# Kernel tuning notes

Measured on AMD Instinct MI355X. Metric: run time of the kernel, lower is better.

Reference implementation:

```python
import jax, jax.numpy as jnp
import numpy as np

N = 100000   # nodes
E = 1600000  # edges
FEAT = 128
HID = 128
TGT = 64
L = 3
G = 512      # graphs in batch


def setup_inputs() -> dict:
    key = jax.random.key(0)
    ks = jax.random.split(key, 16)
    s = 0.05
    return {
        "x": jax.random.normal(ks[0], (N, FEAT), jnp.float32),
        "edge_index": jax.random.randint(ks[1], (2, E), 0, N, dtype=jnp.int32),
        "batch": jnp.sort(jax.random.randint(ks[2], (N,), 0, G, dtype=jnp.int32)),
        "conv_w1": jax.random.normal(ks[3], (L, FEAT, HID), jnp.float32) * s,
        "conv_b1": jax.random.normal(ks[4], (L, HID), jnp.float32) * s,
        "conv_w2": jax.random.normal(ks[5], (L, HID, HID), jnp.float32) * s,
        "conv_b2": jax.random.normal(ks[6], (L, HID), jnp.float32) * s,
        "eps": jnp.zeros((L,), jnp.float32),
        "gn_scale": jnp.ones((L, HID), jnp.float32),
        "gn_weight": jnp.ones((L, HID), jnp.float32),
        "gn_bias": jnp.zeros((L, HID), jnp.float32),
        "proj_w1": jax.random.normal(ks[7], (L, HID, HID), jnp.float32) * s,
        "proj_b1": jax.random.normal(ks[8], (L, HID), jnp.float32) * s,
        "proj_w2": jax.random.normal(ks[9], (L, HID, TGT), jnp.float32) * s,
        "proj_b2": jax.random.normal(ks[10], (L, TGT), jnp.float32) * s,
    }


def _graph_norm(h, batch, counts, scale, weight, bias):
    # per-graph mean -> scatter back to nodes
    mean = jax.ops.segment_sum(h, batch, num_segments=G) / counts
    sub = h - mean[batch] * scale
    var = jax.ops.segment_sum(sub * sub, batch, num_segments=G) / counts
    std = jnp.sqrt(var + 1e-8)
    return weight * sub / std[batch] + bias


def reference(x, edge_index, batch, conv_w1, conv_b1, conv_w2, conv_b2, eps,
              gn_scale, gn_weight, gn_bias, proj_w1, proj_b1, proj_w2, proj_b2):
    src, dst = edge_index[0], edge_index[1]
    counts = jnp.maximum(
        jax.ops.segment_sum(jnp.ones((N, 1), x.dtype), batch, num_segments=G), 1.0)
    h = x
    z_cat = []
    for l in range(L):
        # GINConv: aggr_j->i then 2-layer MLP
        aggr = jax.ops.segment_sum(h[src], dst, num_segments=N)
        h = (1.0 + eps[l]) * h + aggr
        h = jax.nn.relu(h @ conv_w1[l] + conv_b1[l]) @ conv_w2[l] + conv_b2[l]
        # GraphNorm
        h = _graph_norm(h, batch, counts, gn_scale[l], gn_weight[l], gn_bias[l])
        h = jax.nn.relu(h)
        # projection MLP + global add pool
        z = jax.nn.relu(h @ proj_w1[l] + proj_b1[l]) @ proj_w2[l] + proj_b2[l]
        z_cat.append(jax.ops.segment_sum(z, batch, num_segments=G))
    return jnp.concatenate(z_cat, axis=-1)  # [G, L*TGT]
```

## Files before the change

### kernel.cpp

```cpp
#include <hip/hip_runtime.h>

#define NN 100000
#define EE 1600000
#define HIDD 128
#define TGTT 64
#define GGG 512
#define NBK 98
#define CAPB 17408
#define ABLK 200
#define LSTR 136
#define CVTB 3125
#define GBLK 782
#define OUTB 128

typedef unsigned short ushort_t;
typedef __attribute__((ext_vector_type(8))) short short8;
typedef __attribute__((ext_vector_type(4))) float f32x4;
typedef __attribute__((ext_vector_type(4))) unsigned short us4;

__device__ __forceinline__ float b2f(ushort_t u) {
    union { unsigned int i; float f; } v; v.i = ((unsigned int)u) << 16; return v.f;
}
__device__ __forceinline__ ushort_t f2b(float f) {
    union { float f; unsigned int i; } v; v.f = f;
    unsigned int r = (v.i + 0x7fffu + ((v.i >> 16) & 1u)) >> 16;
    return (ushort_t)r;
}

__global__ __launch_bounds__(256) void k_pro(const float* __restrict__ x, ushort_t* __restrict__ Xb,
                                             const float* __restrict__ cw1, const float* __restrict__ cw2,
                                             const float* __restrict__ pw1, ushort_t* __restrict__ Wt,
                                             const int* __restrict__ batch, int* __restrict__ goff,
                                             const int* __restrict__ ei, int* __restrict__ gcnt,
                                             unsigned int* __restrict__ bbuf) {
    __shared__ ushort_t sW[128 * 129];
    __shared__ int cnt[NBK], base[NBK], cur[NBK];
    int b = blockIdx.x, t = threadIdx.x;

    if (b < CVTB) {
        long i0 = (long)b * 1024 + t;
#pragma unroll
        for (int c = 0; c < 4; c++) {
            long i = i0 + c * 256;
            float4 v = ((const float4*)x)[i];
            us4 o; o.x = f2b(v.x); o.y = f2b(v.y); o.z = f2b(v.z); o.w = f2b(v.w);
            ((us4*)Xb)[i] = o;
        }
        return;
    }
    b -= CVTB;
    if (b < 9) {
        int l = b / 3, j = b % 3;
        const float* src = (j == 0 ? cw1 : j == 1 ? cw2 : pw1) + (size_t)l * HIDD * HIDD;
        ushort_t* dst = Wt + (size_t)b * HIDD * HIDD;
        for (int i = t; i < HIDD * HIDD; i += 256) {
            int k = i >> 7, n = i & 127;
            sW[n * 129 + k] = f2b(src[i]);
        }
        __syncthreads();
        for (int i = t; i < HIDD * HIDD; i += 256) {
            dst[i] = sW[(i >> 7) * 129 + (i & 127)];
        }
        return;
    }
    b -= 9;
    if (b < 3) {
        int g = b * 256 + t;
        if (g > GGG) return;
        int lo = 0, hi = NN;
        while (lo < hi) { int mid = (lo + hi) >> 1; if (batch[mid] < g) lo = mid + 1; else hi = mid; }
        goff[g] = lo;
        return;
    }
    b -= 3;
    {
        if (t < NBK) cnt[t] = 0;
        __syncthreads();
        int e0 = b * 8000;
        int e1 = min(e0 + 8000, EE);
        for (int e = e0 + t; e < e1; e += 256)
            atomicAdd(&cnt[ei[EE + e] >> 10], 1);
        __syncthreads();
        if (t < NBK) { base[t] = atomicAdd(&gcnt[t], cnt[t]); cur[t] = 0; }
        __syncthreads();
        for (int e = e0 + t; e < e1; e += 256) {
            int s = ei[e], d = ei[EE + e];
            int bk = d >> 10;
            int off = base[bk] + atomicAdd(&cur[bk], 1);
            if (off < CAPB)
                bbuf[(long)bk * CAPB + off] = (unsigned int)s | (((unsigned int)d & 1023u) << 17);
        }
    }
}

__global__ __launch_bounds__(256) void k_csr(const int* __restrict__ gcnt,
                                             const unsigned int* __restrict__ bbuf,
                                             int* __restrict__ rowptr, int* __restrict__ csr) {
    __shared__ int ldeg[1024], lcur[1024], tsum[256], sb[NBK];
    int b = blockIdx.x, t = threadIdx.x;
    if (t < NBK) sb[t] = gcnt[t];
    __syncthreads();
    if (t == 0) { int a = 0; for (int i = 0; i < NBK; i++) { int v = sb[i]; sb[i] = a; a += v; } }
    __syncthreads();
    int cnt = min(gcnt[b], CAPB);
    int base = sb[b];
    const unsigned int* bb = bbuf + (long)b * CAPB;
#pragma unroll
    for (int i = 0; i < 4; i++) ldeg[t + 256 * i] = 0;
    __syncthreads();
    for (int i = t; i < cnt; i += 256) atomicAdd(&ldeg[bb[i] >> 17], 1);
    __syncthreads();
    int d0 = ldeg[4 * t], d1 = ldeg[4 * t + 1], d2 = ldeg[4 * t + 2], d3 = ldeg[4 * t + 3];
    int tot = d0 + d1 + d2 + d3;
    tsum[t] = tot;
    __syncthreads();
    for (int off = 1; off < 256; off <<= 1) {
        int u = (t >= off) ? tsum[t - off] : 0;
        __syncthreads();
        tsum[t] += u;
        __syncthreads();
    }
    int texcl = tsum[t] - tot;
    int p0 = base + texcl, p1 = p0 + d0, p2 = p1 + d1, p3 = p2 + d2;
    lcur[4 * t] = p0; lcur[4 * t + 1] = p1; lcur[4 * t + 2] = p2; lcur[4 * t + 3] = p3;
    int gnode = b * 1024 + 4 * t;
    if (gnode < NN)     rowptr[gnode]     = p0;
    if (gnode + 1 < NN) rowptr[gnode + 1] = p1;
    if (gnode + 2 < NN) rowptr[gnode + 2] = p2;
    if (gnode + 3 < NN) rowptr[gnode + 3] = p3;
    if (b == NBK - 1 && t == 0) rowptr[NN] = EE;
    __syncthreads();
    for (int i = t; i < cnt; i += 256) {
        unsigned int en = bb[i];
        int pos = atomicAdd(&lcur[en >> 17], 1);
        csr[pos] = (int)(en & 0x1FFFFu);
    }
}

__global__ __launch_bounds__(256) void k_gmlp(const ushort_t* __restrict__ hin,
                                              const int* __restrict__ rowptr,
                                              const int* __restrict__ csr,
                                              const float* __restrict__ eps, int l,
                                              const ushort_t* __restrict__ Wt1, const float* __restrict__ B1,
                                              const ushort_t* __restrict__ Wt2, const float* __restrict__ B2,
                                              ushort_t* __restrict__ Y,
                                              const float* __restrict__ pooledP, const int* __restrict__ goff,
                                              const float* __restrict__ WoP, const float* __restrict__ BoP,
                                              float* __restrict__ outP, int lprev) {
    __shared__ ushort_t sX[128 * LSTR];
    int tid = threadIdx.x;

    if (blockIdx.x >= GBLK) {
        if (lprev < 0) return;
        int ob = blockIdx.x - GBLK;
        int sub = tid >> 6, tt = tid & 63;
        int g = ob * 4 + sub;
        if (g >= GGG) return;
        float cntg = (float)(goff[g + 1] - goff[g]);
        float acc = cntg * BoP[tt];
        const float* p = pooledP + (long)g * HIDD;
        for (int k = 0; k < HIDD; k++) acc += p[k] * WoP[k * TGTT + tt];
        outP[(long)g * (3 * TGTT) + lprev * TGTT + tt] = acc;
        return;
    }

    long base = (long)blockIdx.x * 128;
    int lane = tid & 15, ng = tid >> 4;
    int off = lane << 3;
    float e1 = 1.0f + eps[l];

#pragma unroll 1
    for (int it = 0; it < 8; it++) {
        int row = it * 16 + ng;
        long node = base + row;
        short8 o = (short8)0;
        if (node < NN) {
            short8 h = *(const short8*)(hin + (node << 7) + off);
            float acc[8];
#pragma unroll
            for (int t = 0; t < 8; t++) acc[t] = e1 * b2f((ushort_t)h[t]);
            int jb = rowptr[node], je = rowptr[node + 1];
            int j = jb;
            for (; j + 8 <= je; j += 8) {
                int s0 = csr[j], s1 = csr[j + 1], s2 = csr[j + 2], s3 = csr[j + 3];
                int s4 = csr[j + 4], s5 = csr[j + 5], s6 = csr[j + 6], s7 = csr[j + 7];
                short8 v0 = *(const short8*)(hin + ((long)s0 << 7) + off);
                short8 v1 = *(const short8*)(hin + ((long)s1 << 7) + off);
                short8 v2 = *(const short8*)(hin + ((long)s2 << 7) + off);
                short8 v3 = *(const short8*)(hin + ((long)s3 << 7) + off);
                short8 v4 = *(const short8*)(hin + ((long)s4 << 7) + off);
                short8 v5 = *(const short8*)(hin + ((long)s5 << 7) + off);
                short8 v6 = *(const short8*)(hin + ((long)s6 << 7) + off);
                short8 v7 = *(const short8*)(hin + ((long)s7 << 7) + off);
#pragma unroll
                for (int t = 0; t < 8; t++)
                    acc[t] += ((b2f((ushort_t)v0[t]) + b2f((ushort_t)v1[t])) +
                               (b2f((ushort_t)v2[t]) + b2f((ushort_t)v3[t]))) +
                              ((b2f((ushort_t)v4[t]) + b2f((ushort_t)v5[t])) +
                               (b2f((ushort_t)v6[t]) + b2f((ushort_t)v7[t])));
            }
            for (; j + 4 <= je; j += 4) {
                int s0 = csr[j], s1 = csr[j + 1], s2 = csr[j + 2], s3 = csr[j + 3];
                short8 v0 = *(const short8*)(hin + ((long)s0 << 7) + off);
                short8 v1 = *(const short8*)(hin + ((long)s1 << 7) + off);
                short8 v2 = *(const short8*)(hin + ((long)s2 << 7) + off);
                short8 v3 = *(const short8*)(hin + ((long)s3 << 7) + off);
#pragma unroll
                for (int t = 0; t < 8; t++)
                    acc[t] += (b2f((ushort_t)v0[t]) + b2f((ushort_t)v1[t])) +
                              (b2f((ushort_t)v2[t]) + b2f((ushort_t)v3[t]));
            }
            for (; j < je; j++) {
                int s = csr[j];
                short8 v = *(const short8*)(hin + ((long)s << 7) + off);
#pragma unroll
                for (int t = 0; t < 8; t++) acc[t] += b2f((ushort_t)v[t]);
            }
#pragma unroll
            for (int t = 0; t < 8; t++) o[t] = (short)f2b(acc[t]);
        }
        *(short8*)(sX + row * LSTR + off) = o;
    }
    __syncthreads();

    int w = tid >> 6, l64 = tid & 63, q = l64 >> 4, l16 = l64 & 15;
    int r0 = w * 16, r1 = 64 + w * 16;
    short8 a0[4], a1[4];
#pragma unroll
    for (int c = 0; c < 4; c++) {
        a0[c] = *(const short8*)(sX + (r0 + l16) * LSTR + q * 8 + c * 32);
        a1[c] = *(const short8*)(sX + (r1 + l16) * LSTR + q * 8 + c * 32);
    }
    f32x4 acc0[8], acc1[8];
#pragma unroll
    for (int nt = 0; nt < 8; nt++) {
        int col = nt * 16 + l16;
        float bias = B1[col];
        f32x4 c0 = {bias, bias, bias, bias};
        f32x4 c1 = c0;
        const ushort_t* bB = Wt1 + col * HIDD + q * 8;
#pragma unroll
        for (int c = 0; c < 4; c++) {
            short8 b = *(const short8*)(bB + c * 32);
            c0 = __builtin_amdgcn_mfma_f32_16x16x32_bf16(a0[c], b, c0, 0, 0, 0);
            c1 = __builtin_amdgcn_mfma_f32_16x16x32_bf16(a1[c], b, c1, 0, 0, 0);
        }
        acc0[nt] = c0; acc1[nt] = c1;
    }
    __syncthreads();
#pragma unroll
    for (int nt = 0; nt < 8; nt++) {
        int col = nt * 16 + l16;
#pragma unroll
        for (int r = 0; r < 4; r++) {
            sX[(r0 + q * 4 + r) * LSTR + col] = f2b(fmaxf(acc0[nt][r], 0.f));
            sX[(r1 + q * 4 + r) * LSTR + col] = f2b(fmaxf(acc1[nt][r], 0.f));
        }
    }
    __syncthreads();
#pragma unroll
    for (int c = 0; c < 4; c++) {
        a0[c] = *(const short8*)(sX + (r0 + l16) * LSTR + q * 8 + c * 32);
        a1[c] = *(const short8*)(sX + (r1 + l16) * LSTR + q * 8 + c * 32);
    }
#pragma unroll
    for (int nt = 0; nt < 8; nt++) {
        int col = nt * 16 + l16;
        float bias = B2[col];
        f32x4 c0 = {bias, bias, bias, bias};
        f32x4 c1 = c0;
        const ushort_t* bB = Wt2 + col * HIDD + q * 8;
#pragma unroll
        for (int c = 0; c < 4; c++) {
            short8 b = *(const short8*)(bB + c * 32);
            c0 = __builtin_amdgcn_mfma_f32_16x16x32_bf16(a0[c], b, c0, 0, 0, 0);
            c1 = __builtin_amdgcn_mfma_f32_16x16x32_bf16(a1[c], b, c1, 0, 0, 0);
        }
#pragma unroll
        for (int r = 0; r < 4; r++) {
            long row0 = base + r0 + q * 4 + r;
            long row1 = base + r1 + q * 4 + r;
            if (row0 < NN) Y[(row0 << 7) + col] = f2b(c0[r]);
            if (row1 < NN) Y[(row1 << 7) + col] = f2b(c1[r]);
        }
    }
}

__global__ __launch_bounds__(512) void k_gstat(const ushort_t* __restrict__ Hraw,
                                               const int* __restrict__ goff,
                                               const float* __restrict__ scale,
                                               const float* __restrict__ weight,
                                               float* __restrict__ msb, float* __restrict__ invb,
                                               float* __restrict__ pooled) {
    int g = blockIdx.x;
    int s = goff[g], e = goff[g + 1];
    float cnt = (float)max(e - s, 1);
    int fp = threadIdx.x & 63;
    int r = threadIdx.x >> 6;
    int f0 = fp * 2;
    float s0 = 0.f, s1 = 0.f, q0 = 0.f, q1 = 0.f;
    for (int i = s + r; i < e; i += 8) {
        unsigned int v = *(const unsigned int*)(Hraw + ((long)i << 7) + f0);
        float a = b2f((ushort_t)(v & 0xffffu));
        float b = b2f((ushort_t)(v >> 16));
        s0 += a; q0 += a * a; s1 += b; q1 += b * b;
    }
    __shared__ float red[4][8][64];
    red[0][r][fp] = s0; red[1][r][fp] = q0; red[2][r][fp] = s1; red[3][r][fp] = q1;
    __syncthreads();
    if (r == 0) {
#pragma unroll
        for (int k = 1; k < 8; k++) {
            s0 += red[0][k][fp]; q0 += red[1][k][fp];
            s1 += red[2][k][fp]; q1 += red[3][k][fp];
        }
        float mean0 = s0 / cnt, mean1 = s1 / cnt;
        float ms0 = mean0 * scale[f0], ms1 = mean1 * scale[f0 + 1];
        float var0 = q0 / cnt - 2.f * ms0 * mean0 + ms0 * ms0;
        float var1 = q1 / cnt - 2.f * ms1 * mean1 + ms1 * ms1;
        msb[g * HIDD + f0] = ms0;
        msb[g * HIDD + f0 + 1] = ms1;
        invb[g * HIDD + f0] = weight[f0] / sqrtf(var0 + 1e-8f);
        invb[g * HIDD + f0 + 1] = weight[f0 + 1] / sqrtf(var1 + 1e-8f);
        pooled[g * HIDD + f0] = 0.f;
        pooled[g * HIDD + f0 + 1] = 0.f;
    }
}

__global__ __launch_bounds__(256) void k_projpool(const ushort_t* __restrict__ Hraw,
                                                  const int* __restrict__ batch,
                                                  const float* __restrict__ msb, const float* __restrict__ invb,
                                                  const float* __restrict__ gnb,
                                                  const ushort_t* __restrict__ Wt, const float* __restrict__ B,
                                                  ushort_t* __restrict__ Hn, float* __restrict__ pooled,
                                                  int store_hn) {
    __shared__ ushort_t sX[128 * LSTR];
    __shared__ int sgid[128];
    int tid = threadIdx.x;
    long base = (long)blockIdx.x * 128;
#pragma unroll
    for (int c = 0; c < 8; c++) {
        int idx = c * 256 + tid;
        int row = idx >> 4, cw = idx & 15;
        long grow = base + row;
        short8 v = (short8)0;
        if (grow < NN) {
            short8 raw = *(const short8*)(Hraw + (grow << 7) + (cw << 3));
            int g = batch[grow];
            if (cw == 0) sgid[row] = g;
            const float* msp = msb + g * HIDD + (cw << 3);
            const float* ivp = invb + g * HIDD + (cw << 3);
            const float* gbp = gnb + (cw << 3);
            float4 m0 = *(const float4*)msp, m1 = *(const float4*)(msp + 4);
            float4 i0 = *(const float4*)ivp, i1 = *(const float4*)(ivp + 4);
            float4 g0 = *(const float4*)gbp, g1 = *(const float4*)(gbp + 4);
            float mv[8] = {m0.x, m0.y, m0.z, m0.w, m1.x, m1.y, m1.z, m1.w};
            float iv[8] = {i0.x, i0.y, i0.z, i0.w, i1.x, i1.y, i1.z, i1.w};
            float gv[8] = {g0.x, g0.y, g0.z, g0.w, g1.x, g1.y, g1.z, g1.w};
#pragma unroll
            for (int t = 0; t < 8; t++) {
                float val = (b2f((ushort_t)raw[t]) - mv[t]) * iv[t] + gv[t];
                v[t] = (short)f2b(val > 0.f ? val : 0.f);
            }
            if (store_hn) *(short8*)(Hn + (grow << 7) + (cw << 3)) = v;
        } else if (cw == 0) {
            sgid[row] = -1;
        }
        *(short8*)(sX + row * LSTR + (cw << 3)) = v;
    }
    __syncthreads();

    int w = tid >> 6, l64 = tid & 63, q = l64 >> 4, l16 = l64 & 15;
    int r0 = w * 16, r1 = 64 + w * 16;
    short8 a0[4], a1[4];
#pragma unroll
    for (int c = 0; c < 4; c++) {
        a0[c] = *(const short8*)(sX + (r0 + l16) * LSTR + q * 8 + c * 32);
        a1[c] = *(const short8*)(sX + (r1 + l16) * LSTR + q * 8 + c * 32);
    }
    f32x4 acc0[8], acc1[8];
#pragma unroll
    for (int nt = 0; nt < 8; nt++) {
        int col = nt * 16 + l16;
        float bias = B[col];
        f32x4 c0 = {bias, bias, bias, bias};
        f32x4 c1 = c0;
        const ushort_t* bB = Wt + col * HIDD + q * 8;
#pragma unroll
        for (int c = 0; c < 4; c++) {
            short8 b = *(const short8*)(bB + c * 32);
            c0 = __builtin_amdgcn_mfma_f32_16x16x32_bf16(a0[c], b, c0, 0, 0, 0);
            c1 = __builtin_amdgcn_mfma_f32_16x16x32_bf16(a1[c], b, c1, 0, 0, 0);
        }
        acc0[nt] = c0; acc1[nt] = c1;
    }
    __syncthreads();
#pragma unroll
    for (int nt = 0; nt < 8; nt++) {
        int col = nt * 16 + l16;
#pragma unroll
        for (int r = 0; r < 4; r++) {
            sX[(r0 + q * 4 + r) * LSTR + col] = f2b(fmaxf(acc0[nt][r], 0.f));
            sX[(r1 + q * 4 + r) * LSTR + col] = f2b(fmaxf(acc1[nt][r], 0.f));
        }
    }
    __syncthreads();

    int f = tid & 127, half = tid >> 7;
    int rbeg = half * 64, rend = rbeg + 64;
    float sum = 0.f;
    int curg = -1;
    for (int row = rbeg; row < rend; row++) {
        int g = sgid[row];
        if (g != curg) {
            if (curg >= 0) atomicAdd(&pooled[(long)curg * HIDD + f], sum);
            sum = 0.f; curg = g;
        }
        if (g >= 0) sum += b2f(sX[row * LSTR + f]);
    }
    if (curg >= 0) atomicAdd(&pooled[(long)curg * HIDD + f], sum);
}

__global__ __launch_bounds__(256) void k_out(const float* __restrict__ pooled, const int* __restrict__ goff,
                                             const float* __restrict__ W, const float* __restrict__ B,
                                             float* __restrict__ out, int l) {
    int sub = threadIdx.x >> 6, tt = threadIdx.x & 63;
    int g = blockIdx.x * 4 + sub;
    if (g >= GGG) return;
    float cnt = (float)(goff[g + 1] - goff[g]);
    float acc = cnt * B[tt];
    const float* p = pooled + (long)g * HIDD;
    for (int k = 0; k < HIDD; k++) acc += p[k] * W[k * TGTT + tt];
    out[(long)g * (3 * TGTT) + l * TGTT + tt] = acc;
}

extern "C" void kernel_launch(void* const* d_in, const int* in_sizes, int n_in,
                              void* d_out, int out_size, void* d_ws, size_t ws_size,
                              hipStream_t stream) {
    const float* x    = (const float*)d_in[0];
    const int*   ei   = (const int*)d_in[1];
    const int*   batch= (const int*)d_in[2];
    const float* cw1  = (const float*)d_in[3];
    const float* cb1  = (const float*)d_in[4];
    const float* cw2  = (const float*)d_in[5];
    const float* cb2  = (const float*)d_in[6];
    const float* eps  = (const float*)d_in[7];
    const float* gsc  = (const float*)d_in[8];
    const float* gw   = (const float*)d_in[9];
    const float* gb   = (const float*)d_in[10];
    const float* pw1  = (const float*)d_in[11];
    const float* pb1  = (const float*)d_in[12];
    const float* pw2  = (const float*)d_in[13];
    const float* pb2  = (const float*)d_in[14];
    float* out = (float*)d_out;

    ushort_t* Xb   = (ushort_t*)d_ws;
    ushort_t* Hn   = Xb;
    ushort_t* Hraw = Xb + (size_t)NN * HIDD;
    ushort_t* Wt   = Hraw + (size_t)NN * HIDD;
    float* msb     = (float*)(Wt + (size_t)9 * HIDD * HIDD);
    float* invb    = msb + (size_t)GGG * HIDD;
    float* pooled  = invb + (size_t)GGG * HIDD;
    int* goff   = (int*)(pooled + (size_t)GGG * HIDD);
    int* rowptr = goff + (GGG + 1);
    int* gcnt   = rowptr + (NN + 1);
    int* csr    = gcnt + NBK;
    unsigned int* bbuf = (unsigned int*)(csr + EE);

    hipMemsetAsync(gcnt, 0, NBK * sizeof(int), stream);
    k_pro<<<CVTB + 9 + 3 + ABLK, 256, 0, stream>>>(x, Xb, cw1, cw2, pw1, Wt, batch, goff, ei, gcnt, bbuf);
    k_csr<<<NBK, 256, 0, stream>>>(gcnt, bbuf, rowptr, csr);

    for (int l = 0; l < 3; l++) {
        const ushort_t* hin = (l == 0) ? Xb : Hn;
        ushort_t* Wt1 = Wt + (size_t)(l * 3 + 0) * HIDD * HIDD;
        ushort_t* Wt2 = Wt + (size_t)(l * 3 + 1) * HIDD * HIDD;
        ushort_t* Wtp = Wt + (size_t)(l * 3 + 2) * HIDD * HIDD;
        int grid = GBLK + (l > 0 ? OUTB : 0);
        k_gmlp<<<grid, 256, 0, stream>>>(hin, rowptr, csr, eps, l,
                                         Wt1, cb1 + l * HIDD, Wt2, cb2 + l * HIDD, Hraw,
                                         pooled, goff,
                                         pw2 + (size_t)(l - 1) * HIDD * TGTT, pb2 + (l - 1) * TGTT,
                                         out, l - 1);
        k_gstat<<<GGG, 512, 0, stream>>>(Hraw, goff, gsc + l * HIDD, gw + l * HIDD, msb, invb, pooled);
        k_projpool<<<GBLK, 256, 0, stream>>>(Hraw, batch, msb, invb, gb + l * HIDD,
                                             Wtp, pb1 + l * HIDD, Hn, pooled, (l < 2) ? 1 : 0);
    }
    k_out<<<OUTB, 256, 0, stream>>>(pooled, goff, pw2 + (size_t)2 * HIDD * TGTT, pb2 + 2 * TGTT, out, 2);
}
```

Measured before the change: 614.5 us.

## Double block size to 512 threads and stage weights in shared memory

k_gmlp and k_projpool now run 512 threads per block, so each wave handles one 16-row MFMA tile instead of two. This halves accumulator register pressure and doubles the number of waves available for the latency-bound gather. Weight matrices are also copied into padded shared memory instead of being read from global per wave. The cost is extra shared-memory use per block (about 68 KB in k_gmlp), which may limit how many blocks fit on a CU. The extra output blocks in k_gmlp now handle 8 graphs each, so OUTB drops to 64.

New measurement: 726.7 us. 1.18x slower.

```diff
diff --git a/kernel.cpp b/kernel.cpp
--- a/kernel.cpp
+++ b/kernel.cpp
@@ -9,9 +9,10 @@
 #define CAPB 17408
 #define ABLK 200
 #define LSTR 136
+#define WSTR 132
 #define CVTB 3125
 #define GBLK 782
-#define OUTB 128
+#define OUTB 64
 
 typedef unsigned short ushort_t;
 typedef __attribute__((ext_vector_type(8))) short short8;
@@ -137,24 +138,25 @@
     }
 }
 
-__global__ __launch_bounds__(256) void k_gmlp(const ushort_t* __restrict__ hin,
-                                              const int* __restrict__ rowptr,
-                                              const int* __restrict__ csr,
-                                              const float* __restrict__ eps, int l,
-                                              const ushort_t* __restrict__ Wt1, const float* __restrict__ B1,
-                                              const ushort_t* __restrict__ Wt2, const float* __restrict__ B2,
-                                              ushort_t* __restrict__ Y,
-                                              const float* __restrict__ pooledP, const int* __restrict__ goff,
-                                              const float* __restrict__ WoP, const float* __restrict__ BoP,
-                                              float* __restrict__ outP, int lprev) {
+__global__ __launch_bounds__(512, 4) void k_gmlp(const ushort_t* __restrict__ hin,
+                                                 const int* __restrict__ rowptr,
+                                                 const int* __restrict__ csr,
+                                                 const float* __restrict__ eps, int l,
+                                                 const ushort_t* __restrict__ Wt1, const float* __restrict__ B1,
+                                                 const ushort_t* __restrict__ Wt2, const float* __restrict__ B2,
+                                                 ushort_t* __restrict__ Y,
+                                                 const float* __restrict__ pooledP, const int* __restrict__ goff,
+                                                 const float* __restrict__ WoP, const float* __restrict__ BoP,
+                                                 float* __restrict__ outP, int lprev) {
     __shared__ ushort_t sX[128 * LSTR];
+    __shared__ ushort_t sW[128 * WSTR];
     int tid = threadIdx.x;
 
     if (blockIdx.x >= GBLK) {
         if (lprev < 0) return;
         int ob = blockIdx.x - GBLK;
         int sub = tid >> 6, tt = tid & 63;
-        int g = ob * 4 + sub;
+        int g = ob * 8 + sub;
         if (g >= GGG) return;
         float cntg = (float)(goff[g + 1] - goff[g]);
         float acc = cntg * BoP[tt];
@@ -164,14 +166,21 @@
         return;
     }
 
+#pragma unroll
+    for (int it = 0; it < 4; it++) {
+        int i = it * 512 + tid;
+        int n = i >> 4, kb = i & 15;
+        *(short8*)(sW + n * WSTR + kb * 8) = *(const short8*)(Wt1 + n * HIDD + kb * 8);
+    }
+
     long base = (long)blockIdx.x * 128;
     int lane = tid & 15, ng = tid >> 4;
     int off = lane << 3;
     float e1 = 1.0f + eps[l];
 
 #pragma unroll 1
-    for (int it = 0; it < 8; it++) {
-        int row = it * 16 + ng;
+    for (int it = 0; it < 4; it++) {
+        int row = it * 32 + ng;
         long node = base + row;
         short8 o = (short8)0;
         if (node < NN) {
@@ -224,64 +233,60 @@
     __syncthreads();
 
     int w = tid >> 6, l64 = tid & 63, q = l64 >> 4, l16 = l64 & 15;
-    int r0 = w * 16, r1 = 64 + w * 16;
-    short8 a0[4], a1[4];
-#pragma unroll
-    for (int c = 0; c < 4; c++) {
-        a0[c] = *(const short8*)(sX + (r0 + l16) * LSTR + q * 8 + c * 32);
-        a1[c] = *(const short8*)(sX + (r1 + l16) * LSTR + q * 8 + c * 32);
-    }
-    f32x4 acc0[8], acc1[8];
+    int r0 = w * 16;
+    short8 a[4];
+#pragma unroll
+    for (int c = 0; c < 4; c++)
+        a[c] = *(const short8*)(sX + (r0 + l16) * LSTR + q * 8 + c * 32);
+    f32x4 acc[8];
 #pragma unroll
     for (int nt = 0; nt < 8; nt++) {
         int col = nt * 16 + l16;
         float bias = B1[col];
         f32x4 c0 = {bias, bias, bias, bias};
-        f32x4 c1 = c0;
-        const ushort_t* bB = Wt1 + col * HIDD + q * 8;
+        const ushort_t* bB = sW + col * WSTR + q * 8;
 #pragma unroll
         for (int c = 0; c < 4; c++) {
             short8 b = *(const short8*)(bB + c * 32);
-            c0 = __builtin_amdgcn_mfma_f32_16x16x32_bf16(a0[c], b, c0, 0, 0, 0);
-            c1 = __builtin_amdgcn_mfma_f32_16x16x32_bf16(a1[c], b, c1, 0, 0, 0);
-        }
-        acc0[nt] = c0; acc1[nt] = c1;
-    }
-    __syncthreads();
+            c0 = __builtin_amdgcn_mfma_f32_16x16x32_bf16(a[c], b, c0, 0, 0, 0);
+        }
+        acc[nt] = c0;
+    }
+    __syncthreads();
+
 #pragma unroll
     for (int nt = 0; nt < 8; nt++) {
         int col = nt * 16 + l16;
 #pragma unroll
-        for (int r = 0; r < 4; r++) {
-            sX[(r0 + q * 4 + r) * LSTR + col] = f2b(fmaxf(acc0[nt][r], 0.f));
-            sX[(r1 + q * 4 + r) * LSTR + col] = f2b(fmaxf(acc1[nt][r], 0.f));
-        }
-    }
-    __syncthreads();
-#pragma unroll
-    for (int c = 0; c < 4; c++) {
-        a0[c] = *(const short8*)(sX + (r0 + l16) * LSTR + q * 8 + c * 32);
-        a1[c] = *(const short8*)(sX + (r1 + l16) * LSTR + q * 8 + c * 32);
-    }
+        for (int r = 0; r < 4; r++)
+            sX[(r0 + q * 4 + r) * LSTR + col] = f2b(fmaxf(acc[nt][r], 0.f));
+    }
+#pragma unroll
+    for (int it = 0; it < 4; it++) {
+        int i = it * 512 + tid;
+        int n = i >> 4, kb = i & 15;
+        *(short8*)(sW + n * WSTR + kb * 8) = *(const short8*)(Wt2 + n * HIDD + kb * 8);
+    }
+    __syncthreads();
+
+#pragma unroll
+    for (int c = 0; c < 4; c++)
+        a[c] = *(const short8*)(sX + (r0 + l16) * LSTR + q * 8 + c * 32);
 #pragma unroll
     for (int nt = 0; nt < 8; nt++) {
         int col = nt * 16 + l16;
         float bias = B2[col];
         f32x4 c0 = {bias, bias, bias, bias};
-        f32x4 c1 = c0;
-        const ushort_t* bB = Wt2 + col * HIDD + q * 8;
+        const ushort_t* bB = sW + col * WSTR + q * 8;
 #pragma unroll
         for (int c = 0; c < 4; c++) {
             short8 b = *(const short8*)(bB + c * 32);
-            c0 = __builtin_amdgcn_mfma_f32_16x16x32_bf16(a0[c], b, c0, 0, 0, 0);
-            c1 = __builtin_amdgcn_mfma_f32_16x16x32_bf16(a1[c], b, c1, 0, 0, 0);
+            c0 = __builtin_amdgcn_mfma_f32_16x16x32_bf16(a[c], b, c0, 0, 0, 0);
         }
 #pragma unroll
         for (int r = 0; r < 4; r++) {
-            long row0 = base + r0 + q * 4 + r;
-            long row1 = base + r1 + q * 4 + r;
-            if (row0 < NN) Y[(row0 << 7) + col] = f2b(c0[r]);
-            if (row1 < NN) Y[(row1 << 7) + col] = f2b(c1[r]);
+            long row = base + r0 + q * 4 + r;
+            if (row < NN) Y[(row << 7) + col] = f2b(c0[r]);
         }
     }
 }
@@ -327,20 +332,29 @@
     }
 }
 
-__global__ __launch_bounds__(256) void k_projpool(const ushort_t* __restrict__ Hraw,
-                                                  const int* __restrict__ batch,
-                                                  const float* __restrict__ msb, const float* __restrict__ invb,
-                                                  const float* __restrict__ gnb,
-                                                  const ushort_t* __restrict__ Wt, const float* __restrict__ B,
-                                                  ushort_t* __restrict__ Hn, float* __restrict__ pooled,
-                                                  int store_hn) {
+__global__ __launch_bounds__(512, 4) void k_projpool(const ushort_t* __restrict__ Hraw,
+                                                     const int* __restrict__ batch,
+                                                     const float* __restrict__ msb, const float* __restrict__ invb,
+                                                     const float* __restrict__ gnb,
+                                                     const ushort_t* __restrict__ Wt, const float* __restrict__ B,
+                                                     ushort_t* __restrict__ Hn, float* __restrict__ pooled,
+                                                     int store_hn) {
     __shared__ ushort_t sX[128 * LSTR];
+    __shared__ ushort_t sW[128 * WSTR];
     __shared__ int sgid[128];
     int tid = threadIdx.x;
     long base = (long)blockIdx.x * 128;
-#pragma unroll
-    for (int c = 0; c < 8; c++) {
-        int idx = c * 256 + tid;
+
+#pragma unroll
+    for (int it = 0; it < 4; it++) {
+        int i = it * 512 + tid;
+        int n = i >> 4, kb = i & 15;
+        *(short8*)(sW + n * WSTR + kb * 8) = *(const short8*)(Wt + n * HIDD + kb * 8);
+    }
+
+#pragma unroll
+    for (int c = 0; c < 4; c++) {
+        int idx = c * 512 + tid;
         int row = idx >> 4, cw = idx & 15;
         long grow = base + row;
         short8 v = (short8)0;
@@ -371,43 +385,36 @@
     __syncthreads();
 
     int w = tid >> 6, l64 = tid & 63, q = l64 >> 4, l16 = l64 & 15;
-    int r0 = w * 16, r1 = 64 + w * 16;
-    short8 a0[4], a1[4];
-#pragma unroll
-    for (int c = 0; c < 4; c++) {
-        a0[c] = *(const short8*)(sX + (r0 + l16) * LSTR + q * 8 + c * 32);
-        a1[c] = *(const short8*)(sX + (r1 + l16) * LSTR + q * 8 + c * 32);
-    }
-    f32x4 acc0[8], acc1[8];
+    int r0 = w * 16;
+    short8 a[4];
+#pragma unroll
+    for (int c = 0; c < 4; c++)
+        a[c] = *(const short8*)(sX + (r0 + l16) * LSTR + q * 8 + c * 32);
+    f32x4 acc[8];
 #pragma unroll
     for (int nt = 0; nt < 8; nt++) {
         int col = nt * 16 + l16;
         float bias = B[col];
         f32x4 c0 = {bias, bias, bias, bias};
-        f32x4 c1 = c0;
-        const ushort_t* bB = Wt + col * HIDD + q * 8;
+        const ushort_t* bB = sW + col * WSTR + q * 8;
 #pragma unroll
         for (int c = 0; c < 4; c++) {
             short8 b = *(const short8*)(bB + c * 32);
-            c0 = __builtin_amdgcn_mfma_f32_16x16x32_bf16(a0[c], b, c0, 0, 0, 0);
-            c1 = __builtin_amdgcn_mfma_f32_16x16x32_bf16(a1[c], b, c1, 0, 0, 0);
-        }
-        acc0[nt] = c0; acc1[nt] = c1;
-    }
-    __syncthreads();
+            c0 = __builtin_amdgcn_mfma_f32_16x16x32_bf16(a[c], b, c0, 0, 0, 0);
+        }
+        acc[nt] = c0;
+    }
 #pragma unroll
     for (int nt = 0; nt < 8; nt++) {
         int col = nt * 16 + l16;
 #pragma unroll
-        for (int r = 0; r < 4; r++) {
-            sX[(r0 + q * 4 + r) * LSTR + col] = f2b(fmaxf(acc0[nt][r], 0.f));
-            sX[(r1 + q * 4 + r) * LSTR + col] = f2b(fmaxf(acc1[nt][r], 0.f));
-        }
-    }
-    __syncthreads();
-
-    int f = tid & 127, half = tid >> 7;
-    int rbeg = half * 64, rend = rbeg + 64;
+        for (int r = 0; r < 4; r++)
+            sX[(r0 + q * 4 + r) * LSTR + col] = f2b(fmaxf(acc[nt][r], 0.f));
+    }
+    __syncthreads();
+
+    int f = tid & 127, quarter = tid >> 7;
+    int rbeg = quarter * 32, rend = rbeg + 32;
     float sum = 0.f;
     int curg = -1;
     for (int row = rbeg; row < rend; row++) {
@@ -477,14 +484,14 @@
         ushort_t* Wt2 = Wt + (size_t)(l * 3 + 1) * HIDD * HIDD;
         ushort_t* Wtp = Wt + (size_t)(l * 3 + 2) * HIDD * HIDD;
         int grid = GBLK + (l > 0 ? OUTB : 0);
-        k_gmlp<<<grid, 256, 0, stream>>>(hin, rowptr, csr, eps, l,
+        k_gmlp<<<grid, 512, 0, stream>>>(hin, rowptr, csr, eps, l,
                                          Wt1, cb1 + l * HIDD, Wt2, cb2 + l * HIDD, Hraw,
                                          pooled, goff,
                                          pw2 + (size_t)(l - 1) * HIDD * TGTT, pb2 + (l - 1) * TGTT,
                                          out, l - 1);
         k_gstat<<<GGG, 512, 0, stream>>>(Hraw, goff, gsc + l * HIDD, gw + l * HIDD, msb, invb, pooled);
-        k_projpool<<<GBLK, 256, 0, stream>>>(Hraw, batch, msb, invb, gb + l * HIDD,
+        k_projpool<<<GBLK, 512, 0, stream>>>(Hraw, batch, msb, invb, gb + l * HIDD,
                                              Wtp, pb1 + l * HIDD, Hn, pooled, (l < 2) ? 1 : 0);
     }
-    k_out<<<OUTB, 256, 0, stream>>>(pooled, goff, pw2 + (size_t)2 * HIDD * TGTT, pb2 + 2 * TGTT, out, 2);
-}
+    k_out<<<128, 256, 0, stream>>>(pooled, goff, pw2 + (size_t)2 * HIDD * TGTT, pb2 + 2 * TGTT, out, 2);
+}
```
